# Performance work log

Measured on AMD Instinct MI355X. Metric: run time of the kernel, lower is better.

The kernel has to match this reference:

```python
import jax, jax.numpy as jnp
import numpy as np

V = 32000   # vocab_size
H = 256     # num_hiddens
B = 32      # batch
T = 128     # seq_len


def setup_inputs() -> dict:
    key = jax.random.key(0)
    ks = jax.random.split(key, 10)
    s = 0.05  # keep pre-activations in a sane range
    return {
        "X": jax.random.randint(ks[0], (B, T), 0, V),
        "H0": jnp.zeros((B, H), jnp.float32),
        "Wz": (jax.random.normal(ks[1], (H, V + H)) * s).astype(jnp.float32),
        "bz": (jax.random.normal(ks[2], (H,)) * s).astype(jnp.float32),
        "Wr": (jax.random.normal(ks[3], (H, V + H)) * s).astype(jnp.float32),
        "br": (jax.random.normal(ks[4], (H,)) * s).astype(jnp.float32),
        "Wh": (jax.random.normal(ks[5], (H, V + H)) * s).astype(jnp.float32),
        "bh": (jax.random.normal(ks[6], (H,)) * s).astype(jnp.float32),
        "Wo": (jax.random.normal(ks[7], (V, H)) * s).astype(jnp.float32),
        "bo": (jax.random.normal(ks[8], (V,)) * s).astype(jnp.float32),
    }


def reference(X, H0, Wz, bz, Wr, br, Wh, bh, Wo, bo):
    # nn.Linear(cat(one_hot(x), h)) == gather of the vocab-columns + h @ Wh.T.
    # one_hot(x) @ W[:, :V].T  ==  W[:, :V].T[x]  (row gather), same math, no dense one-hot GEMM.
    vocab = Wo.shape[0]
    Wz_x, Wz_h = Wz[:, :vocab], Wz[:, vocab:]
    Wr_x, Wr_h = Wr[:, :vocab], Wr[:, vocab:]
    Wh_x, Wh_h = Wh[:, :vocab], Wh[:, vocab:]

    Xt = X.T                 # [T, B] -- matches X.T in torch forward
    gz = Wz_x.T[Xt]          # [T, B, H]
    gr = Wr_x.T[Xt]          # [T, B, H]
    gh = Wh_x.T[Xt]          # [T, B, H]

    def step(Hs, g):
        gz_t, gr_t, gh_t = g
        z = jax.nn.sigmoid(gz_t + Hs @ Wz_h.T + bz)
        r = jax.nn.sigmoid(gr_t + Hs @ Wr_h.T + br)
        h = jnp.tanh(gh_t + (r * Hs) @ Wh_h.T + bh)
        Hn = z * h + (1.0 - z) * Hs
        Y = Hn @ Wo.T + bo   # [B, V]
        return Hn, Y

    Hf, Ys = jax.lax.scan(step, H0, (gz, gr, gh))  # Ys: [T, B, V]
    # torch.cat(outputs, dim=0) stacks time-major -> [T*B, V]
    return Ys.reshape(-1, vocab), Hf
```

## Files before the change

kernel.cpp:

```cpp
#include <hip/hip_runtime.h>
#include <hip/hip_fp16.h>
#include <stdint.h>

#define VV 32000
#define HH 256
#define BB 32
#define TT 128
#define VH 32256
#define NTILE 4000

typedef _Float16 f16;
typedef _Float16 f16x2 __attribute__((ext_vector_type(2)));
typedef _Float16 f16x8 __attribute__((ext_vector_type(8)));
typedef float f32x16 __attribute__((ext_vector_type(16)));
typedef unsigned long long u64;

static __device__ __forceinline__ float dot2f(uint32_t w, uint32_t h, float acc){
  f16x2 a = __builtin_bit_cast(f16x2, w);
  f16x2 b = __builtin_bit_cast(f16x2, h);
#if __has_builtin(__builtin_amdgcn_fdot2)
  return __builtin_amdgcn_fdot2(a, b, acc, false);
#else
  acc = fmaf((float)a[0], (float)b[0], acc);
  acc = fmaf((float)a[1], (float)b[1], acc);
  return acc;
#endif
}

__global__ void k_prep(const int* __restrict__ X,
                       const float* __restrict__ Wz, const float* __restrict__ bz,
                       const float* __restrict__ Wr, const float* __restrict__ br,
                       const float* __restrict__ Wh, const float* __restrict__ bh,
                       const float* __restrict__ Wo,
                       float* __restrict__ g_buf, uint32_t* __restrict__ Wpack,
                       f16* __restrict__ Wof, int* __restrict__ ctl){
  const int bid = blockIdx.x;
  const int tidx = threadIdx.x;
  if (bid < 4096){
    int t = bid >> 5, b = bid & 31;
    int tok = X[b*TT + t];
    int o = tidx;
    g_buf[(size_t)bid*768 + o]       = Wz[(size_t)o*VH + tok] + bz[o];
    g_buf[(size_t)bid*768 + 256 + o] = Wr[(size_t)o*VH + tok] + br[o];
    g_buf[(size_t)bid*768 + 512 + o] = Wh[(size_t)o*VH + tok] + bh[o];
  } else if (bid < 4480){
    int idx = (bid - 4096)*256 + tidx;
    int t = idx / 192, rem = idx - t*192;
    int ol = rem >> 4, p = rem & 15;
    int ko = t & 7, no = t >> 3;
    int k = ko*32 + p*2;
    const float* W; int row;
    if (ol < 8){ int o = no*8 + ol; if (o < 256){ W = Wz; row = o; } else { W = Wr; row = o - 256; } }
    else { W = Wh; row = no*4 + (ol - 8); }
    float a = W[(size_t)row*VH + VV + k];
    float c = W[(size_t)row*VH + VV + k + 1];
    f16x2 v; v[0] = (f16)a; v[1] = (f16)c;
    Wpack[idx] = __builtin_bit_cast(uint32_t, v);
  } else if (bid < 8480){
    int i = (bid - 4480)*256 + tidx;
    const float4* s = (const float4*)Wo + (size_t)i*2;
    float4 f0 = s[0], f1 = s[1];
    f16x8 h;
    h[0]=(f16)f0.x; h[1]=(f16)f0.y; h[2]=(f16)f0.z; h[3]=(f16)f0.w;
    h[4]=(f16)f1.x; h[5]=(f16)f1.y; h[6]=(f16)f1.z; h[7]=(f16)f1.w;
    *(f16x8*)(Wof + (size_t)i*8) = h;
  } else {
    for (int i = tidx; i < 4100; i += 256) ctl[i] = 0;
  }
}

#define DECL16(P) uint32_t P##_0,P##_1,P##_2,P##_3,P##_4,P##_5,P##_6,P##_7, \
                           P##_8,P##_9,P##_10,P##_11,P##_12,P##_13,P##_14,P##_15;
#define LDQ(j,e0,e1,e2,e3) { uint4 v_ = src[j]; \
  asm("v_accvgpr_write_b32 %0, %1" : "=a"(e0) : "v"(v_.x)); \
  asm("v_accvgpr_write_b32 %0, %1" : "=a"(e1) : "v"(v_.y)); \
  asm("v_accvgpr_write_b32 %0, %1" : "=a"(e2) : "v"(v_.z)); \
  asm("v_accvgpr_write_b32 %0, %1" : "=a"(e3) : "v"(v_.w)); }
#define LDROW(r,P) LDQ(4*(r)+0,P##_0,P##_1,P##_2,P##_3)   LDQ(4*(r)+1,P##_4,P##_5,P##_6,P##_7) \
                   LDQ(4*(r)+2,P##_8,P##_9,P##_10,P##_11) LDQ(4*(r)+3,P##_12,P##_13,P##_14,P##_15)
#define RD(a_) __extension__({ uint32_t t_; \
  asm volatile("v_accvgpr_read_b32 %0, %1" : "=v"(t_) : "a"(a_)); t_; })
#define DOTP1(p) { \
  uint32_t r0_=RD(w0_##p), r1_=RD(w1_##p), r2_=RD(w2_##p), r3_=RD(w3_##p), \
           r4_=RD(w4_##p), r5_=RD(w5_##p), r6_=RD(w6_##p), r7_=RD(w7_##p); \
  a0 = dot2f(r0_, hp[p], a0); a1 = dot2f(r1_, hp[p], a1); \
  a2 = dot2f(r2_, hp[p], a2); a3 = dot2f(r3_, hp[p], a3); \
  a4 = dot2f(r4_, hp[p], a4); a5 = dot2f(r5_, hp[p], a5); \
  a6 = dot2f(r6_, hp[p], a6); a7 = dot2f(r7_, hp[p], a7); }
#define DOTP2(p) { \
  uint32_t r8_=RD(w8_##p), r9_=RD(w9_##p), r10_=RD(w10_##p), r11_=RD(w11_##p); \
  b0 = dot2f(r8_,  rp[p], b0); b1 = dot2f(r9_,  rp[p], b1); \
  b2 = dot2f(r10_, rp[p], b2); b3 = dot2f(r11_, rp[p], b3); }
#define REDUCE(x) x += __shfl_xor(x,1); x += __shfl_xor(x,2); x += __shfl_xor(x,4);

__global__ __launch_bounds__(512)
__attribute__((amdgpu_waves_per_eu(2, 2)))
void k_main(const float* __restrict__ H0, const uint32_t* __restrict__ Wpack,
            const float* __restrict__ g_buf,
            const f16* __restrict__ Wof, const float* __restrict__ bo,
            f16* __restrict__ Hn16, float* __restrict__ Y, float* __restrict__ hf_out,
            int* __restrict__ ctl){
  __shared__ __align__(16) f16 a_lds[128*128];
  __shared__ __align__(16) f16 b_lds[256*128];
  __shared__ __align__(16) uint32_t hs16[128];
  __shared__ __align__(16) f16 rHs16[256];
  __shared__ __align__(16) u64 hstage[256];
  __shared__ float hs32[256];
  __shared__ float z_s[256];
  __shared__ int sh_role, sh_tile;
  const int tid = threadIdx.x;
  if (tid == 0) sh_role = atomicAdd(&ctl[4096], 1);
  __syncthreads();
  const int role = sh_role;

  if (role < BB){
    const int b = role;
    const int ko = tid & 7, no = tid >> 3;

    DECL16(w0) DECL16(w1) DECL16(w2)  DECL16(w3)  DECL16(w4)  DECL16(w5)
    DECL16(w6) DECL16(w7) DECL16(w8)  DECL16(w9)  DECL16(w10) DECL16(w11)
    {
      const uint4* src = (const uint4*)(Wpack + (size_t)tid*192);
      LDROW(0,w0) LDROW(1,w1) LDROW(2,w2)   LDROW(3,w3)  LDROW(4,w4)  LDROW(5,w5)
      LDROW(6,w6) LDROW(7,w7) LDROW(8,w8)   LDROW(9,w9)  LDROW(10,w10) LDROW(11,w11)
    }

    if (tid < 256) hs32[tid] = H0[b*HH + tid];
    __syncthreads();
    if (tid < 128){
      f16x2 v; v[0] = (f16)hs32[2*tid]; v[1] = (f16)hs32[2*tid+1];
      hs16[tid] = __builtin_bit_cast(uint32_t, v);
    }
    __syncthreads();

    const int gi1 = no*8 + ko;
    const int gi2 = 512 + no*4 + (ko & 3);
    float g1 = g_buf[(size_t)b*768 + gi1];
    float g2 = g_buf[(size_t)b*768 + gi2];
    float g1n = 0.f, g2n = 0.f;

    for (int t = 0; t < TT; t++){
      if (t < TT-1){
        const float* gn = g_buf + (size_t)((t+1)*BB + b)*768;
        g1n = gn[gi1];
        g2n = gn[gi2];
      }

      uint32_t hp[16];
      {
        const uint4* hsp = (const uint4*)hs16;
        #pragma unroll
        for (int j=0;j<4;j++){
          uint4 v = hsp[ko*4 + j];
          hp[4*j] = v.x; hp[4*j+1] = v.y; hp[4*j+2] = v.z; hp[4*j+3] = v.w;
        }
      }
      float a0=0.f,a1=0.f,a2=0.f,a3=0.f,a4=0.f,a5=0.f,a6=0.f,a7=0.f;
      DOTP1(0)  DOTP1(1)  DOTP1(2)  DOTP1(3)  DOTP1(4)  DOTP1(5)  DOTP1(6)  DOTP1(7)
      DOTP1(8)  DOTP1(9)  DOTP1(10) DOTP1(11) DOTP1(12) DOTP1(13) DOTP1(14) DOTP1(15)
      REDUCE(a0) REDUCE(a1) REDUCE(a2) REDUCE(a3) REDUCE(a4) REDUCE(a5) REDUCE(a6) REDUCE(a7)
      {
        float sel = a0;
        sel = (ko==1)?a1:sel; sel = (ko==2)?a2:sel; sel = (ko==3)?a3:sel;
        sel = (ko==4)?a4:sel; sel = (ko==5)?a5:sel; sel = (ko==6)?a6:sel; sel = (ko==7)?a7:sel;
        float pre = sel + g1;
        float s = 1.f / (1.f + __expf(-pre));
        int o = no*8 + ko;
        if (no < 32){
          z_s[o] = s;
        } else {
          int op = o - 256;
          rHs16[op] = (f16)(s * hs32[op]);
        }
      }
      __syncthreads();

      uint32_t rp[16];
      {
        const uint4* rpp = (const uint4*)rHs16;
        #pragma unroll
        for (int j=0;j<4;j++){
          uint4 v = rpp[ko*4 + j];
          rp[4*j] = v.x; rp[4*j+1] = v.y; rp[4*j+2] = v.z; rp[4*j+3] = v.w;
        }
      }
      float b0=0.f,b1=0.f,b2=0.f,b3=0.f;
      DOTP2(0)  DOTP2(1)  DOTP2(2)  DOTP2(3)  DOTP2(4)  DOTP2(5)  DOTP2(6)  DOTP2(7)
      DOTP2(8)  DOTP2(9)  DOTP2(10) DOTP2(11) DOTP2(12) DOTP2(13) DOTP2(14) DOTP2(15)
      REDUCE(b0) REDUCE(b1) REDUCE(b2) REDUCE(b3)
      if (ko < 4){
        float sel = b0;
        sel = (ko==1)?b1:sel; sel = (ko==2)?b2:sel; sel = (ko==3)?b3:sel;
        int o = no*4 + ko;
        float pre = sel + g2;
        float ax = fabsf(pre);
        float e = __expf(2.f*ax);
        float th = 1.f - 2.f/(e + 1.f);
        th = copysignf(th, pre);
        float z = z_s[o];
        float hn = z*th + (1.f - z)*hs32[o];
        hs32[o] = hn;
        ((f16*)hs16)[o] = (f16)hn;
        ((f16*)hstage)[(t&3)*256 + o] = (f16)hn;
        if (t == TT-1) hf_out[b*HH + o] = hn;
      }
      g1 = g1n; g2 = g2n;
      __syncthreads();
      if ((t & 3) == 3 && tid < 64){
        #pragma unroll
        for (int s4 = 0; s4 < 4; s4++){
          int tr = t - 3 + s4;
          u64 v = hstage[s4*64 + tid];
          __hip_atomic_store(((u64*)Hn16) + (((size_t)(tr*BB + b)) << 6) + tid, v,
                             __ATOMIC_RELAXED, __HIP_MEMORY_SCOPE_AGENT);
        }
        asm volatile("s_waitcnt vmcnt(0)" ::: "memory");
        if (tid == 0)
          __hip_atomic_fetch_add(&ctl[t*32], 1, __ATOMIC_RELAXED, __HIP_MEMORY_SCOPE_AGENT);
      }
    }
  }

  {
    const int lane = tid & 63, wid = tid >> 6;
    const int wm = wid & 1, wn = wid >> 1;
    const int arow = tid >> 2, aseg = tid & 3;
    const int brow = tid >> 1, bseg = tid & 1;
    int fenced_t = -1;
    for (;;){
      if (tid == 0) sh_tile = atomicAdd(&ctl[4097], 1);
      __syncthreads();
      const int tile = sh_tile;
      if (tile >= NTILE) break;
      const int mg = tile / 125;
      const int ng = tile - mg*125;
      const int m0 = mg*128, n0 = ng*256;
      const int t_need = mg*4 + 3;
      if (tid == 0 && t_need > fenced_t){
        while (__hip_atomic_load(&ctl[t_need*32], __ATOMIC_RELAXED, __HIP_MEMORY_SCOPE_AGENT) < BB)
          __builtin_amdgcn_s_sleep(16);
        __threadfence();
        fenced_t = t_need;
      }
      __syncthreads();

      f32x16 acc[2][2];
      {
        f32x16 z = {0.f};
        acc[0][0]=z; acc[0][1]=z; acc[1][0]=z; acc[1][1]=z;
      }

      #pragma unroll 1
      for (int kt=0; kt<2; kt++){
        {
          const uint4* asrc = (const uint4*)(Hn16 + (size_t)(m0+arow)*HH + kt*128 + aseg*32);
          #pragma unroll
          for (int j=0;j<4;j++){
            uint4 v = asrc[j];
            int byte = arow*256 + ((aseg*64 + j*16) ^ ((arow&15)<<4));
            *(uint4*)((char*)a_lds + byte) = v;
          }
          const uint4* bsrc = (const uint4*)(Wof + (size_t)(n0+brow)*HH + kt*128 + bseg*64);
          #pragma unroll
          for (int j=0;j<8;j++){
            uint4 v = bsrc[j];
            int byte = brow*256 + ((bseg*128 + j*16) ^ ((brow&15)<<4));
            *(uint4*)((char*)b_lds + byte) = v;
          }
        }
        __syncthreads();
        #pragma unroll
        for (int kk=0; kk<8; kk++){
          const int kbyte = kk*32 + (lane>>5)*16;
          f16x8 af[2], bf[2];
          #pragma unroll
          for (int mi=0;mi<2;mi++){
            int row = wm*64 + mi*32 + (lane&31);
            int byte = row*256 + (kbyte ^ ((row&15)<<4));
            af[mi] = *(const f16x8*)((const char*)a_lds + byte);
          }
          #pragma unroll
          for (int nj=0;nj<2;nj++){
            int nl = wn*64 + nj*32 + (lane&31);
            int byte = nl*256 + (kbyte ^ ((nl&15)<<4));
            bf[nj] = *(const f16x8*)((const char*)b_lds + byte);
          }
          #pragma unroll
          for (int mi=0;mi<2;mi++)
            #pragma unroll
            for (int nj=0;nj<2;nj++)
              acc[mi][nj] = __builtin_amdgcn_mfma_f32_32x32x16_f16(af[mi], bf[nj], acc[mi][nj], 0, 0, 0);
        }
        __syncthreads();
      }
      #pragma unroll
      for (int nj=0;nj<2;nj++){
        const int col = n0 + wn*64 + nj*32 + (lane & 31);
        const float bov = bo[col];
        #pragma unroll
        for (int mi=0;mi<2;mi++){
          const int rbase = m0 + wm*64 + mi*32 + 4*(lane>>5);
          #pragma unroll
          for (int r=0;r<16;r++){
            int row = rbase + (r&3) + 8*(r>>2);
            Y[(size_t)row*VV + col] = acc[mi][nj][r] + bov;
          }
        }
      }
    }
  }
}

extern "C" void kernel_launch(void* const* d_in, const int* in_sizes, int n_in,
                              void* d_out, int out_size, void* d_ws, size_t ws_size,
                              hipStream_t stream){
  const int*   X  = (const int*)d_in[0];
  const float* H0 = (const float*)d_in[1];
  const float* Wz = (const float*)d_in[2];
  const float* bz = (const float*)d_in[3];
  const float* Wr = (const float*)d_in[4];
  const float* br = (const float*)d_in[5];
  const float* Wh = (const float*)d_in[6];
  const float* bh = (const float*)d_in[7];
  const float* Wo = (const float*)d_in[8];
  const float* bo = (const float*)d_in[9];
  float* out = (float*)d_out;

  char* ws = (char*)d_ws;
  int*      ctl   = (int*)ws;
  uint32_t* Wpack = (uint32_t*)(ws + 16512);
  f16*      Hn16  = (f16*)(ws + 409728);
  f16*      Wof   = (f16*)(ws + 2506880);
  float*    g_buf = (float*)(ws + 18890880);

  k_prep<<<8481, 256, 0, stream>>>(X, Wz, bz, Wr, br, Wh, bh, Wo, g_buf, Wpack, Wof, ctl);
  k_main<<<256, 512, 0, stream>>>(H0, Wpack, g_buf, Wof, bo, Hn16, out, out + 131072000LL, ctl);
}
```

Measured before the change: 464.8 us.

## Use MFMA 32x32x16 for recurrent GRU matvecs instead of fdot2 with AGPR weights

Replaces the per-lane fdot2 dot products, which read weights back from AGPRs and reduce with shuffles, with MFMA 32x32x16 f16 instructions. The recurrent weights are repacked in the prep kernel into MFMA B-fragment layout and held in VGPR arrays, and the hidden vector is broadcast as the A operand so only row 0 of the output is used. This removes the accvgpr reads, shuffle reductions and select chains, at the cost of wasting 31 of 32 MFMA rows and needing 192 VGPRs for weight fragments per thread, which may spill.

```diff
diff --git a/kernel.cpp b/kernel.cpp
--- a/kernel.cpp
+++ b/kernel.cpp
@@ -14,18 +14,6 @@
 typedef _Float16 f16x8 __attribute__((ext_vector_type(8)));
 typedef float f32x16 __attribute__((ext_vector_type(16)));
 typedef unsigned long long u64;
-
-static __device__ __forceinline__ float dot2f(uint32_t w, uint32_t h, float acc){
-  f16x2 a = __builtin_bit_cast(f16x2, w);
-  f16x2 b = __builtin_bit_cast(f16x2, h);
-#if __has_builtin(__builtin_amdgcn_fdot2)
-  return __builtin_amdgcn_fdot2(a, b, acc, false);
-#else
-  acc = fmaf((float)a[0], (float)b[0], acc);
-  acc = fmaf((float)a[1], (float)b[1], acc);
-  return acc;
-#endif
-}
 
 __global__ void k_prep(const int* __restrict__ X,
                        const float* __restrict__ Wz, const float* __restrict__ bz,
@@ -45,13 +33,19 @@
     g_buf[(size_t)bid*768 + 512 + o] = Wh[(size_t)o*VH + tok] + bh[o];
   } else if (bid < 4480){
     int idx = (bid - 4096)*256 + tidx;
-    int t = idx / 192, rem = idx - t*192;
-    int ol = rem >> 4, p = rem & 15;
-    int ko = t & 7, no = t >> 3;
-    int k = ko*32 + p*2;
-    const float* W; int row;
-    if (ol < 8){ int o = no*8 + ol; if (o < 256){ W = Wz; row = o; } else { W = Wr; row = o - 256; } }
-    else { W = Wh; row = no*4 + (ol - 8); }
+    int t = idx / 192, j = idx - t*192;
+    int f = j >> 2, dw = j & 3;
+    int w = t >> 6, l = t & 63;
+    const float* W; int row, kf;
+    if (f < 32){
+      kf = (f < 16) ? f : (f - 16);
+      int orow = 64*w + ((f < 16) ? 0 : 32) + (l & 31);
+      if (orow < 256){ W = Wz; row = orow; } else { W = Wr; row = orow - 256; }
+    } else {
+      kf = f - 32;
+      W = Wh; row = 32*w + (l & 31);
+    }
+    int k = kf*16 + ((l >> 5) << 3) + dw*2;
     float a = W[(size_t)row*VH + VV + k];
     float c = W[(size_t)row*VH + VV + k + 1];
     f16x2 v; v[0] = (f16)a; v[1] = (f16)c;
@@ -69,30 +63,6 @@
   }
 }
 
-#define DECL16(P) uint32_t P##_0,P##_1,P##_2,P##_3,P##_4,P##_5,P##_6,P##_7, \
-                           P##_8,P##_9,P##_10,P##_11,P##_12,P##_13,P##_14,P##_15;
-#define LDQ(j,e0,e1,e2,e3) { uint4 v_ = src[j]; \
-  asm("v_accvgpr_write_b32 %0, %1" : "=a"(e0) : "v"(v_.x)); \
-  asm("v_accvgpr_write_b32 %0, %1" : "=a"(e1) : "v"(v_.y)); \
-  asm("v_accvgpr_write_b32 %0, %1" : "=a"(e2) : "v"(v_.z)); \
-  asm("v_accvgpr_write_b32 %0, %1" : "=a"(e3) : "v"(v_.w)); }
-#define LDROW(r,P) LDQ(4*(r)+0,P##_0,P##_1,P##_2,P##_3)   LDQ(4*(r)+1,P##_4,P##_5,P##_6,P##_7) \
-                   LDQ(4*(r)+2,P##_8,P##_9,P##_10,P##_11) LDQ(4*(r)+3,P##_12,P##_13,P##_14,P##_15)
-#define RD(a_) __extension__({ uint32_t t_; \
-  asm volatile("v_accvgpr_read_b32 %0, %1" : "=v"(t_) : "a"(a_)); t_; })
-#define DOTP1(p) { \
-  uint32_t r0_=RD(w0_##p), r1_=RD(w1_##p), r2_=RD(w2_##p), r3_=RD(w3_##p), \
-           r4_=RD(w4_##p), r5_=RD(w5_##p), r6_=RD(w6_##p), r7_=RD(w7_##p); \
-  a0 = dot2f(r0_, hp[p], a0); a1 = dot2f(r1_, hp[p], a1); \
-  a2 = dot2f(r2_, hp[p], a2); a3 = dot2f(r3_, hp[p], a3); \
-  a4 = dot2f(r4_, hp[p], a4); a5 = dot2f(r5_, hp[p], a5); \
-  a6 = dot2f(r6_, hp[p], a6); a7 = dot2f(r7_, hp[p], a7); }
-#define DOTP2(p) { \
-  uint32_t r8_=RD(w8_##p), r9_=RD(w9_##p), r10_=RD(w10_##p), r11_=RD(w11_##p); \
-  b0 = dot2f(r8_,  rp[p], b0); b1 = dot2f(r9_,  rp[p], b1); \
-  b2 = dot2f(r10_, rp[p], b2); b3 = dot2f(r11_, rp[p], b3); }
-#define REDUCE(x) x += __shfl_xor(x,1); x += __shfl_xor(x,2); x += __shfl_xor(x,4);
-
 __global__ __launch_bounds__(512)
 __attribute__((amdgpu_waves_per_eu(2, 2)))
 void k_main(const float* __restrict__ H0, const uint32_t* __restrict__ Wpack,
@@ -102,8 +72,8 @@
             int* __restrict__ ctl){
   __shared__ __align__(16) f16 a_lds[128*128];
   __shared__ __align__(16) f16 b_lds[256*128];
-  __shared__ __align__(16) uint32_t hs16[128];
-  __shared__ __align__(16) f16 rHs16[256];
+  __shared__ __align__(16) f16 hvec[256];
+  __shared__ __align__(16) f16 rH[256];
   __shared__ __align__(16) u64 hstage[256];
   __shared__ float hs32[256];
   __shared__ float z_s[256];
@@ -115,96 +85,89 @@
 
   if (role < BB){
     const int b = role;
-    const int ko = tid & 7, no = tid >> 3;
-
-    DECL16(w0) DECL16(w1) DECL16(w2)  DECL16(w3)  DECL16(w4)  DECL16(w5)
-    DECL16(w6) DECL16(w7) DECL16(w8)  DECL16(w9)  DECL16(w10) DECL16(w11)
+    const int w = tid >> 6, lane = tid & 63;
+
+    f16x8 b0[16], b1[16], b2[16];
     {
       const uint4* src = (const uint4*)(Wpack + (size_t)tid*192);
-      LDROW(0,w0) LDROW(1,w1) LDROW(2,w2)   LDROW(3,w3)  LDROW(4,w4)  LDROW(5,w5)
-      LDROW(6,w6) LDROW(7,w7) LDROW(8,w8)   LDROW(9,w9)  LDROW(10,w10) LDROW(11,w11)
+      #pragma unroll
+      for (int f=0; f<16; f++){
+        b0[f] = __builtin_bit_cast(f16x8, src[f]);
+        b1[f] = __builtin_bit_cast(f16x8, src[16+f]);
+        b2[f] = __builtin_bit_cast(f16x8, src[32+f]);
+      }
     }
 
     if (tid < 256) hs32[tid] = H0[b*HH + tid];
     __syncthreads();
-    if (tid < 128){
-      f16x2 v; v[0] = (f16)hs32[2*tid]; v[1] = (f16)hs32[2*tid+1];
-      hs16[tid] = __builtin_bit_cast(uint32_t, v);
-    }
+    if (tid < 256) hvec[tid] = (f16)hs32[tid];
     __syncthreads();
 
-    const int gi1 = no*8 + ko;
-    const int gi2 = 512 + no*4 + (ko & 3);
-    float g1 = g_buf[(size_t)b*768 + gi1];
-    float g2 = g_buf[(size_t)b*768 + gi2];
-    float g1n = 0.f, g2n = 0.f;
+    const int gi1a = 64*w + (lane & 31);
+    const int gi1b = gi1a + 32;
+    const int gi2  = 512 + 32*w + (lane & 31);
+    float g1a = g_buf[(size_t)b*768 + gi1a];
+    float g1b = g_buf[(size_t)b*768 + gi1b];
+    float g2  = g_buf[(size_t)b*768 + gi2];
+    float g1an = 0.f, g1bn = 0.f, g2n = 0.f;
+
+    const int afoff = (lane >> 5) * 16;
 
     for (int t = 0; t < TT; t++){
       if (t < TT-1){
         const float* gn = g_buf + (size_t)((t+1)*BB + b)*768;
-        g1n = gn[gi1];
-        g2n = gn[gi2];
-      }
-
-      uint32_t hp[16];
-      {
-        const uint4* hsp = (const uint4*)hs16;
-        #pragma unroll
-        for (int j=0;j<4;j++){
-          uint4 v = hsp[ko*4 + j];
-          hp[4*j] = v.x; hp[4*j+1] = v.y; hp[4*j+2] = v.z; hp[4*j+3] = v.w;
-        }
-      }
-      float a0=0.f,a1=0.f,a2=0.f,a3=0.f,a4=0.f,a5=0.f,a6=0.f,a7=0.f;
-      DOTP1(0)  DOTP1(1)  DOTP1(2)  DOTP1(3)  DOTP1(4)  DOTP1(5)  DOTP1(6)  DOTP1(7)
-      DOTP1(8)  DOTP1(9)  DOTP1(10) DOTP1(11) DOTP1(12) DOTP1(13) DOTP1(14) DOTP1(15)
-      REDUCE(a0) REDUCE(a1) REDUCE(a2) REDUCE(a3) REDUCE(a4) REDUCE(a5) REDUCE(a6) REDUCE(a7)
-      {
-        float sel = a0;
-        sel = (ko==1)?a1:sel; sel = (ko==2)?a2:sel; sel = (ko==3)?a3:sel;
-        sel = (ko==4)?a4:sel; sel = (ko==5)?a5:sel; sel = (ko==6)?a6:sel; sel = (ko==7)?a7:sel;
-        float pre = sel + g1;
-        float s = 1.f / (1.f + __expf(-pre));
-        int o = no*8 + ko;
-        if (no < 32){
-          z_s[o] = s;
-        } else {
-          int op = o - 256;
-          rHs16[op] = (f16)(s * hs32[op]);
-        }
+        g1an = gn[gi1a]; g1bn = gn[gi1b]; g2n = gn[gi2];
+      }
+
+      f32x16 acc = {0.f};
+      #pragma unroll
+      for (int kf=0; kf<16; kf++){
+        f16x8 af = *(const f16x8*)((const char*)hvec + kf*32 + afoff);
+        acc = __builtin_amdgcn_mfma_f32_32x32x16_f16(af, b0[kf], acc, 0, 0, 0);
+      }
+      if (lane < 32){
+        int o = 64*w + lane;
+        float p = acc[0] + g1a;
+        float s = 1.f / (1.f + __expf(-p));
+        if (w < 4) z_s[o] = s;
+        else { int ob = o - 256; rH[ob] = (f16)(s * hs32[ob]); }
+      }
+      acc = (f32x16){0.f};
+      #pragma unroll
+      for (int kf=0; kf<16; kf++){
+        f16x8 af = *(const f16x8*)((const char*)hvec + kf*32 + afoff);
+        acc = __builtin_amdgcn_mfma_f32_32x32x16_f16(af, b1[kf], acc, 0, 0, 0);
+      }
+      if (lane < 32){
+        int o = 64*w + 32 + lane;
+        float p = acc[0] + g1b;
+        float s = 1.f / (1.f + __expf(-p));
+        if (w < 4) z_s[o] = s;
+        else { int ob = o - 256; rH[ob] = (f16)(s * hs32[ob]); }
       }
       __syncthreads();
 
-      uint32_t rp[16];
-      {
-        const uint4* rpp = (const uint4*)rHs16;
-        #pragma unroll
-        for (int j=0;j<4;j++){
-          uint4 v = rpp[ko*4 + j];
-          rp[4*j] = v.x; rp[4*j+1] = v.y; rp[4*j+2] = v.z; rp[4*j+3] = v.w;
-        }
-      }
-      float b0=0.f,b1=0.f,b2=0.f,b3=0.f;
-      DOTP2(0)  DOTP2(1)  DOTP2(2)  DOTP2(3)  DOTP2(4)  DOTP2(5)  DOTP2(6)  DOTP2(7)
-      DOTP2(8)  DOTP2(9)  DOTP2(10) DOTP2(11) DOTP2(12) DOTP2(13) DOTP2(14) DOTP2(15)
-      REDUCE(b0) REDUCE(b1) REDUCE(b2) REDUCE(b3)
-      if (ko < 4){
-        float sel = b0;
-        sel = (ko==1)?b1:sel; sel = (ko==2)?b2:sel; sel = (ko==3)?b3:sel;
-        int o = no*4 + ko;
-        float pre = sel + g2;
+      acc = (f32x16){0.f};
+      #pragma unroll
+      for (int kf=0; kf<16; kf++){
+        f16x8 af = *(const f16x8*)((const char*)rH + kf*32 + afoff);
+        acc = __builtin_amdgcn_mfma_f32_32x32x16_f16(af, b2[kf], acc, 0, 0, 0);
+      }
+      if (lane < 32){
+        int o2 = 32*w + lane;
+        float pre = acc[0] + g2;
         float ax = fabsf(pre);
         float e = __expf(2.f*ax);
         float th = 1.f - 2.f/(e + 1.f);
         th = copysignf(th, pre);
-        float z = z_s[o];
-        float hn = z*th + (1.f - z)*hs32[o];
-        hs32[o] = hn;
-        ((f16*)hs16)[o] = (f16)hn;
-        ((f16*)hstage)[(t&3)*256 + o] = (f16)hn;
-        if (t == TT-1) hf_out[b*HH + o] = hn;
-      }
-      g1 = g1n; g2 = g2n;
+        float z = z_s[o2];
+        float hn = z*th + (1.f - z)*hs32[o2];
+        hs32[o2] = hn;
+        hvec[o2] = (f16)hn;
+        ((f16*)hstage)[(t&3)*256 + o2] = (f16)hn;
+        if (t == TT-1) hf_out[b*HH + o2] = hn;
+      }
+      g1a = g1an; g1b = g1bn; g2 = g2n;
       __syncthreads();
       if ((t & 3) == 3 && tid < 64){
         #pragma unroll
```

New measurement: 731.3 us. +57.4%, slower.
